# Kernel optimization log

Measured on AMD Instinct MI355X. Metric: run time of the kernel, lower is better.

## Reference

```python
import jax, jax.numpy as jnp
import numpy as np
import math

DROPOUT_P = 0.1

def setup_inputs() -> dict:
    key = jax.random.key(0)
    k1, k2, k3 = jax.random.split(key, 3)
    B, Lq, Lk, D = 8, 2048, 2048, 128
    x1 = jax.random.normal(k1, (B, Lq, D), dtype=jnp.float32)
    x2 = jax.random.normal(k2, (B, Lk, D), dtype=jnp.float32)
    qm = jnp.zeros((1, Lq, Lk), dtype=jnp.float32)  # additive attention mask
    u = jax.random.uniform(k3, (B, Lq, Lk), dtype=jnp.float32)  # dropout uniforms
    return {"x1": x1, "x2": x2, "qm": qm, "u": u}

def reference(x1, x2, qm, u):
    # scaled dot-product attention with additive mask + inverted dropout
    scale = 1.0 / math.sqrt(x1.shape[-1])
    qk = jnp.einsum('bqd,bkd->bqk', x1, x2) * scale + qm  # [B, Lq, Lk]
    attn = jax.nn.softmax(qk, axis=-1)
    keep = (u >= DROPOUT_P).astype(attn.dtype) / (1.0 - DROPOUT_P)
    attn = attn * keep
    out = jnp.einsum('bqk,bkd->bqd', attn, x2)  # [B, Lq, D]
    return out
```

## Files before the change

kernel.cpp:

```cpp
#include <hip/hip_runtime.h>
#include <hip/hip_bf16.h>
#include <stdint.h>

#define LQ 2048
#define LK 2048
#define DH 128
#define BQ 32
#define KB 128
#define NT (LK / KB)
#define KROWE 136
#define LOG2E 1.44269504088896340736f
#define QSCALE 0.088388347648318447f

typedef __attribute__((ext_vector_type(8)))  short bf16x8;
typedef __attribute__((ext_vector_type(16))) float f32x16;
typedef __attribute__((ext_vector_type(4)))  float f32x4;

typedef __attribute__((address_space(1))) const void glob_cv;
typedef __attribute__((address_space(3))) void lds_v;

union FragAB { uint32_t u[4]; bf16x8 v; };

__device__ __forceinline__ uint32_t pack2_bf16(float lo, float hi) {
  union { __hip_bfloat16 b; uint16_t u; } a, c;
  a.b = __float2bfloat16(lo);
  c.b = __float2bfloat16(hi);
  return (uint32_t)a.u | ((uint32_t)c.u << 16);
}

__global__ __launch_bounds__(256)
void prep_kernel(const float* __restrict__ x2, uint16_t* __restrict__ Kp,
                 uint16_t* __restrict__ Vp) {
  __shared__ uint16_t tl[128][130];
  const int b = blockIdx.x & 7, tile = blockIdx.x >> 3;
  const int t = threadIdx.x;
  const int row0 = t >> 1, half = t & 1;

  const float* src = x2 + ((size_t)(b * 2048 + tile * 128 + row0)) * 128 + half * 64;
  uint32_t wbuf[32];
#pragma unroll
  for (int i = 0; i < 16; ++i) {
    f32x4 v = *(const f32x4*)(src + i * 4);
    wbuf[2 * i]     = pack2_bf16(v.x, v.y);
    wbuf[2 * i + 1] = pack2_bf16(v.z, v.w);
  }
  uint16_t* kdst = Kp + ((size_t)(b * 2048 + tile * 128 + row0)) * 128 + half * 64;
#pragma unroll
  for (int i = 0; i < 8; ++i)
    *(uint4*)(kdst + i * 8) = *(const uint4*)&wbuf[i * 4];
#pragma unroll
  for (int i = 0; i < 32; ++i)
    *(uint32_t*)&tl[row0][half * 64 + 2 * i] = wbuf[i];
  __syncthreads();

  const int d = t >> 1, halfk = t & 1;
  uint32_t vw[32];
#pragma unroll
  for (int i = 0; i < 32; ++i) {
    const int k = halfk * 64 + 2 * i;
    vw[i] = (uint32_t)tl[k][d] | ((uint32_t)tl[k + 1][d] << 16);
  }
  uint16_t* vdst = Vp + ((size_t)(b * 128 + d)) * 2048 + tile * 128 + halfk * 64;
#pragma unroll
  for (int i = 0; i < 8; ++i)
    *(uint4*)(vdst + i * 8) = *(const uint4*)&vw[i * 4];
}

__global__ __launch_bounds__(256)
void qmt_kernel(const float* __restrict__ qm, uint16_t* __restrict__ qmt2) {
  const int kc = threadIdx.x & 63;
  const int q  = blockIdx.x * 4 + (threadIdx.x >> 6);
  f32x4 r[8];
  const float* src = qm + (size_t)q * 2048 + kc * 32;
#pragma unroll
  for (int c = 0; c < 8; ++c) r[c] = *(const f32x4*)(src + c * 4);
#pragma unroll
  for (int h = 0; h < 2; ++h) {
    uint32_t w[8];
#pragma unroll
    for (int i = 0; i < 8; ++i) {
      const int gi0 = 2 * i, gi1 = 2 * i + 1;
      const float v0 = r[h + (gi0 >> 2) * 2][gi0 & 3] * LOG2E;
      const float v1 = r[h + (gi1 >> 2) * 2][gi1 & 3] * LOG2E;
      w[i] = pack2_bf16(v0, v1);
    }
    uint16_t* dst = qmt2 + ((size_t)(kc * 2 + h) * 2048 + q) * 16;
    uint4 lo = {w[0], w[1], w[2], w[3]};
    uint4 hi = {w[4], w[5], w[6], w[7]};
    *(uint4*)dst = lo;
    *(uint4*)(dst + 8) = hi;
  }
}

__global__ __launch_bounds__(256, 2)
void fattn_kernel(const float* __restrict__ x1,
                  const uint16_t* __restrict__ Kp,
                  const uint16_t* __restrict__ Vp,
                  const float* __restrict__ uu,
                  const uint16_t* __restrict__ qmt2,
                  float* __restrict__ out)
{
  __shared__ char lds[69632];
  uint16_t* lds16 = (uint16_t*)lds;

  const int tid  = threadIdx.x;
  const int wv   = tid >> 6;
  const int lane = tid & 63;
  const int ln   = lane & 31;
  const int h    = lane >> 5;
  const int ks   = wv;

  const int b     = blockIdx.x & 7;
  const int qblk  = blockIdx.x >> 3;
  const int qbase = qblk * BQ;
  const int qrow  = qbase + ln;

  FragAB qf[8];
  {
    const float* qp = x1 + ((size_t)(b * LQ + qrow)) * DH + h * 8;
    const float qs = QSCALE * LOG2E;
#pragma unroll
    for (int dc = 0; dc < 8; ++dc) {
      f32x4 a = *(const f32x4*)(qp + dc * 16);
      f32x4 c = *(const f32x4*)(qp + dc * 16 + 4);
      qf[dc].u[0] = pack2_bf16(a.x * qs, a.y * qs);
      qf[dc].u[1] = pack2_bf16(a.z * qs, a.w * qs);
      qf[dc].u[2] = pack2_bf16(c.x * qs, c.y * qs);
      qf[dc].u[3] = pack2_bf16(c.z * qs, c.w * qs);
    }
  }

  int koffs[9], voffs[9];
#pragma unroll
  for (int jj = 0; jj < 9; ++jj) {
    const int j = jj * 4 + wv;
    if (j < 34) {
      const int G = j * 64 + lane;
      const int row = (G * 61681) >> 20;
      const int s0  = G - row * 17;
      const int s   = (s0 < 16) ? s0 : 0;
      koffs[jj] = row * 256  + s * 16;
      voffs[jj] = row * 4096 + s * 16;
    } else { koffs[jj] = 0; voffs[jj] = 0; }
  }
  const char* Kpb = (const char*)(Kp + (size_t)b * 2048 * 128);
  const char* Vpb = (const char*)(Vp + (size_t)b * 128 * 2048);

  const float* ub = uu + ((size_t)(b * LQ + qbase + h)) * LK + ks * 32 + ln;

#pragma unroll
  for (int jj = 0; jj < 9; ++jj) {
    const int j = jj * 4 + wv;
    if (j < 34) {
      __builtin_amdgcn_global_load_lds((glob_cv*)(Kpb + koffs[jj]),
                                       (lds_v*)(lds + j * 1024), 16, 0, 0);
      __builtin_amdgcn_global_load_lds((glob_cv*)(Vpb + voffs[jj]),
                                       (lds_v*)(lds + 34816 + j * 1024), 16, 0, 0);
    }
  }

  float ucur[16];
#pragma unroll
  for (int i = 0; i < 16; ++i)
    ucur[i] = __builtin_nontemporal_load(ub + (size_t)(2 * i) * LK);

  uint4 qc0, qc1;
  {
    const uint16_t* qp16 = qmt2 + (((size_t)ks * 2 + h) * 2048 + qrow) * 16;
    qc0 = *(const uint4*)qp16;
    qc1 = *(const uint4*)(qp16 + 8);
  }
  __syncthreads();

  float m_run = -1e30f, l_run = 0.f;
  f32x16 acco[4];
#pragma unroll
  for (int d2 = 0; d2 < 4; ++d2)
#pragma unroll
    for (int i = 0; i < 16; ++i) acco[d2][i] = 0.f;

  for (int t = 0; t < NT; ++t) {
    float unxt[16]; uint4 qn0, qn1;
    if (t + 1 < NT) {
#pragma unroll
      for (int i = 0; i < 16; ++i)
        unxt[i] = __builtin_nontemporal_load(ub + (size_t)((t + 1) * KB) + (size_t)(2 * i) * LK);
      const uint16_t* qp16 = qmt2 + (((size_t)((t + 1) * 4 + ks) * 2 + h) * 2048 + qrow) * 16;
      qn0 = *(const uint4*)qp16;
      qn1 = *(const uint4*)(qp16 + 8);
    }

    f32x16 sacc;
#pragma unroll
    for (int i = 0; i < 16; ++i) sacc[i] = 0.f;
    const uint16_t* Krow = lds16 + (size_t)(ks * 32 + ln) * KROWE + h * 8;
    __builtin_amdgcn_s_setprio(1);
#pragma unroll
    for (int dc = 0; dc < 8; ++dc) {
      bf16x8 af = *(const bf16x8*)(Krow + dc * 16);
      sacc = __builtin_amdgcn_mfma_f32_32x32x16_bf16(af, qf[dc].v, sacc, 0, 0, 0);
    }
    __builtin_amdgcn_s_setprio(0);

#define ADDQM(W, I) { sacc[I] += __uint_as_float((W) << 16); \
                      sacc[I + 1] += __uint_as_float((W) & 0xffff0000u); }
    ADDQM(qc0.x, 0)  ADDQM(qc0.y, 2)  ADDQM(qc0.z, 4)  ADDQM(qc0.w, 6)
    ADDQM(qc1.x, 8)  ADDQM(qc1.y, 10) ADDQM(qc1.z, 12) ADDQM(qc1.w, 14)
#undef ADDQM

    float pm = sacc[0];
#pragma unroll
    for (int i = 1; i < 16; ++i) pm = fmaxf(pm, sacc[i]);
    pm = fmaxf(pm, __shfl_xor(pm, 32));
    const float mnew = fmaxf(m_run, pm);
    const float resc = __builtin_amdgcn_exp2f(m_run - mnew);
    m_run = mnew;
    float rs = 0.f;
#pragma unroll
    for (int i = 0; i < 16; ++i) {
      sacc[i] = __builtin_amdgcn_exp2f(sacc[i] - mnew);
      rs += sacc[i];
    }
    rs += __shfl_xor(rs, 32);
    l_run = l_run * resc + rs;

    uint32_t M = 0;
#pragma unroll
    for (int i = 0; i < 16; ++i) {
      unsigned long long bi = __ballot(ucur[i] >= 0.1f);
      uint32_t sel = (ln & 1) ? (uint32_t)(bi >> 32) : (uint32_t)bi;
      M = ((ln >> 1) == i) ? sel : M;
    }
#pragma unroll
    for (int g = 0; g < 4; ++g)
#pragma unroll
      for (int j2 = 0; j2 < 4; ++j2) {
        const uint32_t keep = (M >> (h * 4 + g * 8 + j2)) & 1u;
        sacc[g * 4 + j2] = keep ? sacc[g * 4 + j2] : 0.f;
      }

    uint32_t pr[4][2], sw[4][2];
#pragma unroll
    for (int g = 0; g < 4; ++g) {
      pr[g][0] = pack2_bf16(sacc[4 * g + 0], sacc[4 * g + 1]);
      pr[g][1] = pack2_bf16(sacc[4 * g + 2], sacc[4 * g + 3]);
      sw[g][0] = __shfl_xor(pr[g][0], 32);
      sw[g][1] = __shfl_xor(pr[g][1], 32);
    }
    FragAB bfr[2];
#pragma unroll
    for (int c = 0; c < 2; ++c) {
      bfr[c].u[0] = h ? sw[2 * c + 1][0] : pr[2 * c][0];
      bfr[c].u[1] = h ? sw[2 * c + 1][1] : pr[2 * c][1];
      bfr[c].u[2] = h ? pr[2 * c + 1][0] : sw[2 * c][0];
      bfr[c].u[3] = h ? pr[2 * c + 1][1] : sw[2 * c][1];
    }

#pragma unroll
    for (int d2 = 0; d2 < 4; ++d2)
#pragma unroll
      for (int i = 0; i < 16; ++i) acco[d2][i] *= resc;

    __builtin_amdgcn_s_setprio(1);
#pragma unroll
    for (int d2 = 0; d2 < 4; ++d2) {
      const uint16_t* Vrow = lds16 + 17408 + (size_t)(d2 * 32 + ln) * KROWE + ks * 32 + h * 8;
#pragma unroll
      for (int c = 0; c < 2; ++c) {
        bf16x8 av = *(const bf16x8*)(Vrow + c * 16);
        acco[d2] = __builtin_amdgcn_mfma_f32_32x32x16_bf16(av, bfr[c].v, acco[d2], 0, 0, 0);
      }
    }
    __builtin_amdgcn_s_setprio(0);

    __syncthreads();
    if (t + 1 < NT) {
      const char* kp = Kpb + (size_t)(t + 1) * 32768;
      const char* vp = Vpb + (size_t)(t + 1) * 256;
#pragma unroll
      for (int jj = 0; jj < 9; ++jj) {
        const int j = jj * 4 + wv;
        if (j < 34) {
          __builtin_amdgcn_global_load_lds((glob_cv*)(kp + koffs[jj]),
                                           (lds_v*)(lds + j * 1024), 16, 0, 0);
          __builtin_amdgcn_global_load_lds((glob_cv*)(vp + voffs[jj]),
                                           (lds_v*)(lds + 34816 + j * 1024), 16, 0, 0);
        }
      }
#pragma unroll
      for (int i = 0; i < 16; ++i) ucur[i] = unxt[i];
      qc0 = qn0; qc1 = qn1;
      __syncthreads();
    }
  }

  float* scr = (float*)lds + (size_t)wv * 4224;
  scr[lane]      = m_run;
  scr[64 + lane] = l_run;
#pragma unroll
  for (int d2 = 0; d2 < 4; ++d2)
#pragma unroll
    for (int g = 0; g < 4; ++g) {
      f32x4 vv;
#pragma unroll
      for (int j2 = 0; j2 < 4; ++j2) vv[j2] = acco[d2][g * 4 + j2];
      *(f32x4*)(scr + 128 + (size_t)(d2 * 4 + g) * 256 + lane * 4) = vv;
    }
  __syncthreads();

  if (wv < 2) {
    const float* rg[4];
#pragma unroll
    for (int s2 = 0; s2 < 4; ++s2) rg[s2] = (const float*)lds + (size_t)s2 * 4224;
    const float ms0 = rg[0][lane], ms1 = rg[1][lane], ms2 = rg[2][lane], ms3 = rg[3][lane];
    const float ls0 = rg[0][64 + lane], ls1 = rg[1][64 + lane];
    const float ls2 = rg[2][64 + lane], ls3 = rg[3][64 + lane];
    const float mM = fmaxf(fmaxf(ms0, ms1), fmaxf(ms2, ms3));
    const float e0 = __builtin_amdgcn_exp2f(ms0 - mM);
    const float e1 = __builtin_amdgcn_exp2f(ms1 - mM);
    const float e2 = __builtin_amdgcn_exp2f(ms2 - mM);
    const float e3 = __builtin_amdgcn_exp2f(ms3 - mM);
    const float lM = e0 * ls0 + e1 * ls1 + e2 * ls2 + e3 * ls3;
    const float inv = (1.0f / 0.9f) / lM;
    float* op = out + ((size_t)(b * LQ + qbase + ln)) * DH;
#pragma unroll
    for (int dd = 0; dd < 2; ++dd) {
      const int d2 = wv * 2 + dd;
#pragma unroll
      for (int g = 0; g < 4; ++g) {
        const size_t off = 128 + (size_t)(d2 * 4 + g) * 256 + lane * 4;
        f32x4 a4 = e0 * *(const f32x4*)(rg[0] + off)
                 + e1 * *(const f32x4*)(rg[1] + off)
                 + e2 * *(const f32x4*)(rg[2] + off)
                 + e3 * *(const f32x4*)(rg[3] + off);
        a4 = a4 * inv;
        *(f32x4*)(op + d2 * 32 + 8 * g + 4 * h) = a4;
      }
    }
  }
}

extern "C" void kernel_launch(void* const* d_in, const int* in_sizes, int n_in,
                              void* d_out, int out_size, void* d_ws, size_t ws_size,
                              hipStream_t stream) {
  (void)in_sizes; (void)n_in; (void)out_size; (void)ws_size;
  const float* x1 = (const float*)d_in[0];
  const float* x2 = (const float*)d_in[1];
  const float* qm = (const float*)d_in[2];
  const float* u  = (const float*)d_in[3];
  float* out = (float*)d_out;

  uint16_t* qmt2 = (uint16_t*)d_ws;
  uint16_t* Kp   = (uint16_t*)((char*)d_ws + (8u  << 20));
  uint16_t* Vp   = (uint16_t*)((char*)d_ws + (12u << 20));

  prep_kernel<<<dim3(128), dim3(256), 0, stream>>>(x2, Kp, Vp);
  qmt_kernel<<<dim3(512), dim3(256), 0, stream>>>(qm, qmt2);
  fattn_kernel<<<dim3(512), dim3(256), 0, stream>>>(x1, Kp, Vp, u, qmt2, out);
}
```

Measured before the change: 248.8 us.

## Load K/V fragments directly from global and split keys contiguously per wave

Removes the LDS staging of K and V tiles and the per-tile block barriers. Each wave now owns a contiguous 512-key slice and reads its MFMA operand fragments straight from global memory into registers. It also adds a lazy softmax rescale that only updates the running max when a new tile's max exceeds the old one by more than 8, and spreads the final reduction over all four waves. The trade is that K/V reuse across waves through LDS is lost, so more global/L2 traffic and exposed load latency without prefetch are traded for fewer barriers and less LDS traffic.

```diff
diff --git a/kernel.cpp b/kernel.cpp
--- a/kernel.cpp
+++ b/kernel.cpp
@@ -6,18 +6,13 @@
 #define LK 2048
 #define DH 128
 #define BQ 32
-#define KB 128
-#define NT (LK / KB)
-#define KROWE 136
+#define NT 16
 #define LOG2E 1.44269504088896340736f
 #define QSCALE 0.088388347648318447f
 
 typedef __attribute__((ext_vector_type(8)))  short bf16x8;
 typedef __attribute__((ext_vector_type(16))) float f32x16;
 typedef __attribute__((ext_vector_type(4)))  float f32x4;
-
-typedef __attribute__((address_space(1))) const void glob_cv;
-typedef __attribute__((address_space(3))) void lds_v;
 
 union FragAB { uint32_t u[4]; bf16x8 v; };
 
@@ -100,15 +95,13 @@
                   const uint16_t* __restrict__ qmt2,
                   float* __restrict__ out)
 {
-  __shared__ char lds[69632];
-  uint16_t* lds16 = (uint16_t*)lds;
+  __shared__ float scr[4][4224];
 
   const int tid  = threadIdx.x;
-  const int wv   = tid >> 6;
+  const int ks   = tid >> 6;
   const int lane = tid & 63;
   const int ln   = lane & 31;
   const int h    = lane >> 5;
-  const int ks   = wv;
 
   const int b     = blockIdx.x & 7;
   const int qblk  = blockIdx.x >> 3;
@@ -130,34 +123,9 @@
     }
   }
 
-  int koffs[9], voffs[9];
-#pragma unroll
-  for (int jj = 0; jj < 9; ++jj) {
-    const int j = jj * 4 + wv;
-    if (j < 34) {
-      const int G = j * 64 + lane;
-      const int row = (G * 61681) >> 20;
-      const int s0  = G - row * 17;
-      const int s   = (s0 < 16) ? s0 : 0;
-      koffs[jj] = row * 256  + s * 16;
-      voffs[jj] = row * 4096 + s * 16;
-    } else { koffs[jj] = 0; voffs[jj] = 0; }
-  }
-  const char* Kpb = (const char*)(Kp + (size_t)b * 2048 * 128);
-  const char* Vpb = (const char*)(Vp + (size_t)b * 128 * 2048);
-
-  const float* ub = uu + ((size_t)(b * LQ + qbase + h)) * LK + ks * 32 + ln;
-
-#pragma unroll
-  for (int jj = 0; jj < 9; ++jj) {
-    const int j = jj * 4 + wv;
-    if (j < 34) {
-      __builtin_amdgcn_global_load_lds((glob_cv*)(Kpb + koffs[jj]),
-                                       (lds_v*)(lds + j * 1024), 16, 0, 0);
-      __builtin_amdgcn_global_load_lds((glob_cv*)(Vpb + voffs[jj]),
-                                       (lds_v*)(lds + 34816 + j * 1024), 16, 0, 0);
-    }
-  }
+  const uint16_t* Kb = Kp + (size_t)(b * 2048 + ks * 512) * 128;
+  const uint16_t* Vb = Vp + (size_t)b * 128 * 2048 + ks * 512;
+  const float*    ub = uu + ((size_t)(b * LQ + qbase + h)) * LK + ks * 512 + ln;
 
   float ucur[16];
 #pragma unroll
@@ -166,11 +134,10 @@
 
   uint4 qc0, qc1;
   {
-    const uint16_t* qp16 = qmt2 + (((size_t)ks * 2 + h) * 2048 + qrow) * 16;
+    const uint16_t* qp16 = qmt2 + (((size_t)(ks * 16) * 2 + h) * 2048 + qrow) * 16;
     qc0 = *(const uint4*)qp16;
     qc1 = *(const uint4*)(qp16 + 8);
   }
-  __syncthreads();
 
   float m_run = -1e30f, l_run = 0.f;
   f32x16 acco[4];
@@ -180,12 +147,26 @@
     for (int i = 0; i < 16; ++i) acco[d2][i] = 0.f;
 
   for (int t = 0; t < NT; ++t) {
+    const uint16_t* Krow = Kb + (size_t)(t * 32 + ln) * 128 + h * 8;
+    bf16x8 kf[8];
+#pragma unroll
+    for (int dc = 0; dc < 8; ++dc)
+      kf[dc] = *(const bf16x8*)(Krow + dc * 16);
+
+    bf16x8 vf[8];
+#pragma unroll
+    for (int d2 = 0; d2 < 4; ++d2)
+#pragma unroll
+      for (int c = 0; c < 2; ++c)
+        vf[d2 * 2 + c] = *(const bf16x8*)(Vb + (size_t)(d2 * 32 + ln) * 2048 +
+                                          t * 32 + c * 16 + h * 8);
+
     float unxt[16]; uint4 qn0, qn1;
     if (t + 1 < NT) {
 #pragma unroll
       for (int i = 0; i < 16; ++i)
-        unxt[i] = __builtin_nontemporal_load(ub + (size_t)((t + 1) * KB) + (size_t)(2 * i) * LK);
-      const uint16_t* qp16 = qmt2 + (((size_t)((t + 1) * 4 + ks) * 2 + h) * 2048 + qrow) * 16;
+        unxt[i] = __builtin_nontemporal_load(ub + (t + 1) * 32 + (size_t)(2 * i) * LK);
+      const uint16_t* qp16 = qmt2 + (((size_t)(ks * 16 + t + 1) * 2 + h) * 2048 + qrow) * 16;
       qn0 = *(const uint4*)qp16;
       qn1 = *(const uint4*)(qp16 + 8);
     }
@@ -193,13 +174,10 @@
     f32x16 sacc;
 #pragma unroll
     for (int i = 0; i < 16; ++i) sacc[i] = 0.f;
-    const uint16_t* Krow = lds16 + (size_t)(ks * 32 + ln) * KROWE + h * 8;
     __builtin_amdgcn_s_setprio(1);
 #pragma unroll
-    for (int dc = 0; dc < 8; ++dc) {
-      bf16x8 af = *(const bf16x8*)(Krow + dc * 16);
-      sacc = __builtin_amdgcn_mfma_f32_32x32x16_bf16(af, qf[dc].v, sacc, 0, 0, 0);
-    }
+    for (int dc = 0; dc < 8; ++dc)
+      sacc = __builtin_amdgcn_mfma_f32_32x32x16_bf16(kf[dc], qf[dc].v, sacc, 0, 0, 0);
     __builtin_amdgcn_s_setprio(0);
 
 #define ADDQM(W, I) { sacc[I] += __uint_as_float((W) << 16); \
@@ -212,17 +190,24 @@
 #pragma unroll
     for (int i = 1; i < 16; ++i) pm = fmaxf(pm, sacc[i]);
     pm = fmaxf(pm, __shfl_xor(pm, 32));
-    const float mnew = fmaxf(m_run, pm);
-    const float resc = __builtin_amdgcn_exp2f(m_run - mnew);
-    m_run = mnew;
+    if (!__all(pm <= m_run + 8.f)) {
+      const float mnew = fmaxf(m_run, pm);
+      const float resc = __builtin_amdgcn_exp2f(m_run - mnew);
+      l_run *= resc;
+#pragma unroll
+      for (int d2 = 0; d2 < 4; ++d2)
+#pragma unroll
+        for (int i = 0; i < 16; ++i) acco[d2][i] *= resc;
+      m_run = mnew;
+    }
     float rs = 0.f;
 #pragma unroll
     for (int i = 0; i < 16; ++i) {
-      sacc[i] = __builtin_amdgcn_exp2f(sacc[i] - mnew);
+      sacc[i] = __builtin_amdgcn_exp2f(sacc[i] - m_run);
       rs += sacc[i];
     }
     rs += __shfl_xor(rs, 32);
-    l_run = l_run * resc + rs;
+    l_run += rs;
 
     uint32_t M = 0;
 #pragma unroll
@@ -256,47 +241,25 @@
       bfr[c].u[3] = h ? pr[2 * c + 1][1] : sw[2 * c][1];
     }
 
+    __builtin_amdgcn_s_setprio(1);
 #pragma unroll
     for (int d2 = 0; d2 < 4; ++d2)
 #pragma unroll
-      for (int i = 0; i < 16; ++i) acco[d2][i] *= resc;
-
-    __builtin_amdgcn_s_setprio(1);
-#pragma unroll
-    for (int d2 = 0; d2 < 4; ++d2) {
-      const uint16_t* Vrow = lds16 + 17408 + (size_t)(d2 * 32 + ln) * KROWE + ks * 32 + h * 8;
-#pragma unroll
-      for (int c = 0; c < 2; ++c) {
-        bf16x8 av = *(const bf16x8*)(Vrow + c * 16);
-        acco[d2] = __builtin_amdgcn_mfma_f32_32x32x16_bf16(av, bfr[c].v, acco[d2], 0, 0, 0);
-      }
-    }
+      for (int c = 0; c < 2; ++c)
+        acco[d2] = __builtin_amdgcn_mfma_f32_32x32x16_bf16(vf[d2 * 2 + c], bfr[c].v,
+                                                           acco[d2], 0, 0, 0);
     __builtin_amdgcn_s_setprio(0);
 
-    __syncthreads();
     if (t + 1 < NT) {
-      const char* kp = Kpb + (size_t)(t + 1) * 32768;
-      const char* vp = Vpb + (size_t)(t + 1) * 256;
-#pragma unroll
-      for (int jj = 0; jj < 9; ++jj) {
-        const int j = jj * 4 + wv;
-        if (j < 34) {
-          __builtin_amdgcn_global_load_lds((glob_cv*)(kp + koffs[jj]),
-                                           (lds_v*)(lds + j * 1024), 16, 0, 0);
-          __builtin_amdgcn_global_load_lds((glob_cv*)(vp + voffs[jj]),
-                                           (lds_v*)(lds + 34816 + j * 1024), 16, 0, 0);
-        }
-      }
 #pragma unroll
       for (int i = 0; i < 16; ++i) ucur[i] = unxt[i];
       qc0 = qn0; qc1 = qn1;
-      __syncthreads();
-    }
-  }
-
-  float* scr = (float*)lds + (size_t)wv * 4224;
-  scr[lane]      = m_run;
-  scr[64 + lane] = l_run;
+    }
+  }
+
+  float* s = scr[ks];
+  s[lane]      = m_run;
+  s[64 + lane] = l_run;
 #pragma unroll
   for (int d2 = 0; d2 < 4; ++d2)
 #pragma unroll
@@ -304,17 +267,15 @@
       f32x4 vv;
 #pragma unroll
       for (int j2 = 0; j2 < 4; ++j2) vv[j2] = acco[d2][g * 4 + j2];
-      *(f32x4*)(scr + 128 + (size_t)(d2 * 4 + g) * 256 + lane * 4) = vv;
+      *(f32x4*)(s + 128 + (size_t)(d2 * 4 + g) * 256 + lane * 4) = vv;
     }
   __syncthreads();
 
-  if (wv < 2) {
-    const float* rg[4];
-#pragma unroll
-    for (int s2 = 0; s2 < 4; ++s2) rg[s2] = (const float*)lds + (size_t)s2 * 4224;
-    const float ms0 = rg[0][lane], ms1 = rg[1][lane], ms2 = rg[2][lane], ms3 = rg[3][lane];
-    const float ls0 = rg[0][64 + lane], ls1 = rg[1][64 + lane];
-    const float ls2 = rg[2][64 + lane], ls3 = rg[3][64 + lane];
+  {
+    const float ms0 = scr[0][lane], ms1 = scr[1][lane];
+    const float ms2 = scr[2][lane], ms3 = scr[3][lane];
+    const float ls0 = scr[0][64 + lane], ls1 = scr[1][64 + lane];
+    const float ls2 = scr[2][64 + lane], ls3 = scr[3][64 + lane];
     const float mM = fmaxf(fmaxf(ms0, ms1), fmaxf(ms2, ms3));
     const float e0 = __builtin_amdgcn_exp2f(ms0 - mM);
     const float e1 = __builtin_amdgcn_exp2f(ms1 - mM);
@@ -323,19 +284,16 @@
     const float lM = e0 * ls0 + e1 * ls1 + e2 * ls2 + e3 * ls3;
     const float inv = (1.0f / 0.9f) / lM;
     float* op = out + ((size_t)(b * LQ + qbase + ln)) * DH;
-#pragma unroll
-    for (int dd = 0; dd < 2; ++dd) {
-      const int d2 = wv * 2 + dd;
-#pragma unroll
-      for (int g = 0; g < 4; ++g) {
-        const size_t off = 128 + (size_t)(d2 * 4 + g) * 256 + lane * 4;
-        f32x4 a4 = e0 * *(const f32x4*)(rg[0] + off)
-                 + e1 * *(const f32x4*)(rg[1] + off)
-                 + e2 * *(const f32x4*)(rg[2] + off)
-                 + e3 * *(const f32x4*)(rg[3] + off);
-        a4 = a4 * inv;
-        *(f32x4*)(op + d2 * 32 + 8 * g + 4 * h) = a4;
-      }
+    const int d2 = ks;
+#pragma unroll
+    for (int g = 0; g < 4; ++g) {
+      const size_t off = 128 + (size_t)(d2 * 4 + g) * 256 + lane * 4;
+      f32x4 a4 = e0 * *(const f32x4*)(scr[0] + off)
+               + e1 * *(const f32x4*)(scr[1] + off)
+               + e2 * *(const f32x4*)(scr[2] + off)
+               + e3 * *(const f32x4*)(scr[3] + off);
+      a4 = a4 * inv;
+      *(f32x4*)(op + d2 * 32 + 8 * g + 4 * h) = a4;
     }
   }
 }
```

Result: slower. 273.0 us (+9.7%).
